# Performance work log

Hardware: AMD Instinct MI355X
Metric: run time of the kernel (lower is better)

The kernel has to match this reference:

```python
import jax, jax.numpy as jnp
import numpy as np

ALPHA = 1.0


def setup_inputs() -> dict:
    key = jax.random.key(0)
    k1, k2 = jax.random.split(key)
    N, K, D = 131072, 512, 512
    inputs = jax.random.normal(k1, (N, D), dtype=jnp.float32)
    # xavier-uniform style init for clusters
    limit = float(np.sqrt(6.0 / (K + D)))
    clusters = jax.random.uniform(k2, (K, D), dtype=jnp.float32, minval=-limit, maxval=limit)
    return {"inputs": inputs, "clusters": clusters}


def reference(inputs, clusters):
    # (same math as sum((x[:,None,:]-c)**2, -1), without the N x K x D intermediate)
    x2 = jnp.sum(inputs * inputs, axis=1, keepdims=True)          # [N, 1]
    c2 = jnp.sum(clusters * clusters, axis=1)[None, :]            # [1, K]
    d2 = jnp.maximum(x2 + c2 - 2.0 * (inputs @ clusters.T), 0.0)  # [N, K]
    q = 1.0 / (1.0 + d2 / ALPHA)
    q = q ** ((ALPHA + 1.0) / 2.0)
    return q / jnp.sum(q, axis=1, keepdims=True)
```

## Files before the change

kernel.cpp:

```cpp
#include <hip/hip_runtime.h>
#include <stdint.h>

#define NPTS 131072
#define DIM  512
#define KC   512
#define BM   32
#define BK   16
#define NKT  32

typedef float f32x16 __attribute__((ext_vector_type(16)));
typedef float f32x4  __attribute__((ext_vector_type(4)));
typedef float f32x2  __attribute__((ext_vector_type(2)));
typedef short bf16x8 __attribute__((ext_vector_type(8)));
typedef short bf16x2 __attribute__((ext_vector_type(2)));

__device__ __forceinline__ short f2bf(float f) {
  union { float f; unsigned u; } v; v.f = f;
  unsigned r = v.u + 0x7FFFu + ((v.u >> 16) & 1u);
  return (short)(r >> 16);
}

__device__ __forceinline__ bf16x8 pack8(f32x4 a, f32x4 b) {
  bf16x8 p;
  p[0] = f2bf(a.x); p[1] = f2bf(a.y); p[2] = f2bf(a.z); p[3] = f2bf(a.w);
  p[4] = f2bf(b.x); p[5] = f2bf(b.y); p[6] = f2bf(b.z); p[7] = f2bf(b.w);
  return p;
}

__device__ __forceinline__ float sq4(f32x4 a) {
  return a.x*a.x + a.y*a.y + a.z*a.z + a.w*a.w;
}

__device__ __forceinline__ void gload_lds16(const short* g, short* l) {
  __builtin_amdgcn_global_load_lds(
      (const __attribute__((address_space(1))) unsigned int*)g,
      (__attribute__((address_space(3))) unsigned int*)l, 16, 0, 0);
}

__global__ void dec_pack(const float* __restrict__ C, short* __restrict__ Bp,
                         float* __restrict__ c2) {
  const int n    = blockIdx.x;
  const int lane = threadIdx.x;
  const float* src = C + (size_t)n * DIM + lane * 8;
  f32x4 v0 = *(const f32x4*)src;
  f32x4 v1 = *(const f32x4*)(src + 4);
  float s = sq4(v0) + sq4(v1);
  #pragma unroll
  for (int m = 1; m < 64; m <<= 1) s += __shfl_xor(s, m, 64);
  if (lane == 0) c2[n] = s;
  const int kt = lane >> 1;
  const int h  = lane & 1;
  const int wn = n >> 7, nt = (n >> 5) & 3, r = n & 31;
  const size_t slot = ((size_t)(kt * 4 + wn) * 4 + nt) * 64 + h * 32 + r;
  *(bf16x8*)(Bp + slot * 8) = pack8(v0, v1);
}

__global__ __launch_bounds__(256, 4)
void dec_main(const float* __restrict__ X, const short* __restrict__ Bp,
              const float* __restrict__ c2g, float* __restrict__ out) {
  __shared__ short Bbuf[2][KC * BK];
  __shared__ short Abuf[2][BM * BK];
  __shared__ float x2sh[BM];
  __shared__ float part[4][BM];
  __shared__ float rowinv[BM];

  const int tid  = threadIdx.x;
  const int lane = tid & 63;
  const int wn   = tid >> 6;
  const int l31  = lane & 31;
  const int h    = lane >> 5;
  const int row0 = blockIdx.x * BM;

  const int arow = tid >> 3;
  const int acol = tid & 7;
  const float* aptr = X + (size_t)(row0 + arow) * DIM + acol * 2;
  const int awoff = (((acol >> 2) * 32 + arow) << 3) + ((acol & 3) << 1);

  const short* bsrc = Bp + tid * 8;

  f32x16 acc[4];
  #pragma unroll
  for (int nt = 0; nt < 4; ++nt) acc[nt] = (f32x16)0.f;
  float x2a = 0.f;

  {
    #pragma unroll
    for (int sw = 0; sw < 4; ++sw)
      gload_lds16(bsrc + sw * 2048, &Bbuf[0][sw * 2048 + tid * 8]);
    f32x2 a0 = *(const f32x2*)(aptr);
    x2a += a0.x * a0.x + a0.y * a0.y;
    bf16x2 p; p[0] = f2bf(a0.x); p[1] = f2bf(a0.y);
    *(bf16x2*)&Abuf[0][awoff] = p;
  }
  f32x2 av_w = *(const f32x2*)(aptr + 1 * BK);
  f32x2 av_p = *(const f32x2*)(aptr + 2 * BK);
  __syncthreads();

  #pragma unroll 2
  for (int kt = 0; kt < NKT; ++kt) {
    const int cur = kt & 1, nxt = cur ^ 1;

    if (kt + 1 < NKT) {
      #pragma unroll
      for (int sw = 0; sw < 4; ++sw)
        gload_lds16(bsrc + (size_t)(kt + 1) * 8192 + sw * 2048,
                    &Bbuf[nxt][sw * 2048 + tid * 8]);
      x2a += av_w.x * av_w.x + av_w.y * av_w.y;
      bf16x2 p; p[0] = f2bf(av_w.x); p[1] = f2bf(av_w.y);
      *(bf16x2*)&Abuf[nxt][awoff] = p;
      av_w = av_p;
      const int kpre = (kt + 3 < NKT) ? (kt + 3) : (NKT - 1);
      av_p = *(const f32x2*)(aptr + kpre * BK);
    }

    bf16x8 af = *(const bf16x8*)&Abuf[cur][lane * 8];
    bf16x8 bfr[4];
    #pragma unroll
    for (int nt = 0; nt < 4; ++nt)
      bfr[nt] = *(const bf16x8*)&Bbuf[cur][(wn * 4 + nt) * 512 + lane * 8];

    #pragma unroll
    for (int nt = 0; nt < 4; ++nt)
      acc[nt] = __builtin_amdgcn_mfma_f32_32x32x16_bf16(af, bfr[nt], acc[nt], 0, 0, 0);

    __syncthreads();
  }

  x2a += __shfl_xor(x2a, 1, 64);
  x2a += __shfl_xor(x2a, 2, 64);
  x2a += __shfl_xor(x2a, 4, 64);
  if ((tid & 7) == 0) x2sh[arow] = x2a;
  __syncthreads();

  float c2v[4];
  #pragma unroll
  for (int nt = 0; nt < 4; ++nt) c2v[nt] = c2g[wn * 128 + nt * 32 + l31];

  float srow[16];
  #pragma unroll
  for (int r = 0; r < 16; ++r) {
    const int row = (r & 3) + 8 * (r >> 2) + 4 * h;
    const float x2m = x2sh[row];
    float s = 0.f;
    #pragma unroll
    for (int nt = 0; nt < 4; ++nt) {
      float d2 = fmaxf(x2m + c2v[nt] - 2.f * acc[nt][r], 0.f);
      float q = __builtin_amdgcn_rcpf(1.f + d2);
      acc[nt][r] = q;
      s += q;
    }
    #pragma unroll
    for (int msk = 1; msk < 32; msk <<= 1) s += __shfl_xor(s, msk, 64);
    srow[r] = s;
  }

  if (l31 == 0) {
    #pragma unroll
    for (int r = 0; r < 16; ++r)
      part[wn][(r & 3) + 8 * (r >> 2) + 4 * h] = srow[r];
  }
  __syncthreads();
  if (tid < BM)
    rowinv[tid] = __builtin_amdgcn_rcpf(part[0][tid] + part[1][tid] +
                                        part[2][tid] + part[3][tid]);
  __syncthreads();

  #pragma unroll
  for (int r = 0; r < 16; ++r) {
    const int row = (r & 3) + 8 * (r >> 2) + 4 * h;
    const float iv = rowinv[row];
    float* o = out + (size_t)(row0 + row) * KC + wn * 128 + l31;
    #pragma unroll
    for (int nt = 0; nt < 4; ++nt)
      o[nt * 32] = acc[nt][r] * iv;
  }
}

extern "C" void kernel_launch(void* const* d_in, const int* in_sizes, int n_in,
                              void* d_out, int out_size, void* d_ws, size_t ws_size,
                              hipStream_t stream) {
  const float* X = (const float*)d_in[0];
  const float* C = (const float*)d_in[1];
  float* out = (float*)d_out;

  short* Bp = (short*)d_ws;
  float* c2 = (float*)((char*)d_ws + (size_t)KC * DIM * 2);

  dec_pack<<<KC, 64, 0, stream>>>(C, Bp, c2);
  dec_main<<<NPTS / BM, 256, 0, stream>>>(X, Bp, c2, out);
}
```

Measured before the change: 203.4 us.

## Double row tile and K step with 8 waves sharing each cluster tile

Raises the block tile from 32 to 64 rows using 512 threads arranged as 2x4 waves, so each staged cluster tile in LDS feeds twice as many rows. The K step doubles to 32 (two MFMA sub-steps per iteration), which halves the number of barriers. The packed cluster layout and the A-tile layout are reworked to match, and X loads become 16-byte vectors. LDS per block doubles to about 64KB, which may reduce occupancy below the launch-bounds target.

```diff
diff --git a/kernel.cpp b/kernel.cpp
--- a/kernel.cpp
+++ b/kernel.cpp
@@ -4,15 +4,14 @@
 #define NPTS 131072
 #define DIM  512
 #define KC   512
-#define BM   32
-#define BK   16
-#define NKT  32
+#define BM   64
+#define BK   32
+#define NKT  16
 
 typedef float f32x16 __attribute__((ext_vector_type(16)));
 typedef float f32x4  __attribute__((ext_vector_type(4)));
-typedef float f32x2  __attribute__((ext_vector_type(2)));
 typedef short bf16x8 __attribute__((ext_vector_type(8)));
-typedef short bf16x2 __attribute__((ext_vector_type(2)));
+typedef short bf16x4 __attribute__((ext_vector_type(4)));
 
 __device__ __forceinline__ short f2bf(float f) {
   union { float f; unsigned u; } v; v.f = f;
@@ -24,6 +23,12 @@
   bf16x8 p;
   p[0] = f2bf(a.x); p[1] = f2bf(a.y); p[2] = f2bf(a.z); p[3] = f2bf(a.w);
   p[4] = f2bf(b.x); p[5] = f2bf(b.y); p[6] = f2bf(b.z); p[7] = f2bf(b.w);
+  return p;
+}
+
+__device__ __forceinline__ bf16x4 pack4(f32x4 a) {
+  bf16x4 p;
+  p[0] = f2bf(a.x); p[1] = f2bf(a.y); p[2] = f2bf(a.z); p[3] = f2bf(a.w);
   return p;
 }
 
@@ -48,33 +53,38 @@
   #pragma unroll
   for (int m = 1; m < 64; m <<= 1) s += __shfl_xor(s, m, 64);
   if (lane == 0) c2[n] = s;
-  const int kt = lane >> 1;
-  const int h  = lane & 1;
+  const int kt = lane >> 2;
+  const int st = (lane >> 1) & 1;
+  const int hh = lane & 1;
   const int wn = n >> 7, nt = (n >> 5) & 3, r = n & 31;
-  const size_t slot = ((size_t)(kt * 4 + wn) * 4 + nt) * 64 + h * 32 + r;
+  const size_t slot =
+      (((size_t)(kt * 2 + st) * 4 + wn) * 4 + nt) * 64 + hh * 32 + r;
   *(bf16x8*)(Bp + slot * 8) = pack8(v0, v1);
 }
 
-__global__ __launch_bounds__(256, 4)
+__global__ __launch_bounds__(512, 4)
 void dec_main(const float* __restrict__ X, const short* __restrict__ Bp,
               const float* __restrict__ c2g, float* __restrict__ out) {
   __shared__ short Bbuf[2][KC * BK];
-  __shared__ short Abuf[2][BM * BK];
+  __shared__ short Abuf[2][2 * 2 * BM * 8];
   __shared__ float x2sh[BM];
   __shared__ float part[4][BM];
   __shared__ float rowinv[BM];
 
   const int tid  = threadIdx.x;
   const int lane = tid & 63;
-  const int wn   = tid >> 6;
+  const int wave = tid >> 6;
+  const int wm   = wave >> 2;
+  const int wn   = wave & 3;
   const int l31  = lane & 31;
   const int h    = lane >> 5;
   const int row0 = blockIdx.x * BM;
 
   const int arow = tid >> 3;
-  const int acol = tid & 7;
-  const float* aptr = X + (size_t)(row0 + arow) * DIM + acol * 2;
-  const int awoff = (((acol >> 2) * 32 + arow) << 3) + ((acol & 3) << 1);
+  const int ac   = tid & 7;
+  const float* aptr = X + (size_t)(row0 + arow) * DIM + ac * 4;
+  const int awoff = (((ac >> 2) * 2 + ((ac >> 1) & 1)) * BM + arow) * 8 +
+                    (ac & 1) * 4;
 
   const short* bsrc = Bp + tid * 8;
 
@@ -86,42 +96,45 @@
   {
     #pragma unroll
     for (int sw = 0; sw < 4; ++sw)
-      gload_lds16(bsrc + sw * 2048, &Bbuf[0][sw * 2048 + tid * 8]);
-    f32x2 a0 = *(const f32x2*)(aptr);
-    x2a += a0.x * a0.x + a0.y * a0.y;
-    bf16x2 p; p[0] = f2bf(a0.x); p[1] = f2bf(a0.y);
-    *(bf16x2*)&Abuf[0][awoff] = p;
-  }
-  f32x2 av_w = *(const f32x2*)(aptr + 1 * BK);
-  f32x2 av_p = *(const f32x2*)(aptr + 2 * BK);
-  __syncthreads();
-
-  #pragma unroll 2
+      gload_lds16(bsrc + sw * 4096, &Bbuf[0][sw * 4096 + tid * 8]);
+    f32x4 a0 = *(const f32x4*)(aptr);
+    x2a += sq4(a0);
+    *(bf16x4*)&Abuf[0][awoff] = pack4(a0);
+  }
+  f32x4 av_w = *(const f32x4*)(aptr + 1 * BK);
+  f32x4 av_p = *(const f32x4*)(aptr + 2 * BK);
+  __syncthreads();
+
   for (int kt = 0; kt < NKT; ++kt) {
     const int cur = kt & 1, nxt = cur ^ 1;
 
     if (kt + 1 < NKT) {
+      const int kpre = (kt + 3 < NKT) ? (kt + 3) : (NKT - 1);
+      f32x4 av_n = *(const f32x4*)(aptr + kpre * BK);
       #pragma unroll
       for (int sw = 0; sw < 4; ++sw)
-        gload_lds16(bsrc + (size_t)(kt + 1) * 8192 + sw * 2048,
-                    &Bbuf[nxt][sw * 2048 + tid * 8]);
-      x2a += av_w.x * av_w.x + av_w.y * av_w.y;
-      bf16x2 p; p[0] = f2bf(av_w.x); p[1] = f2bf(av_w.y);
-      *(bf16x2*)&Abuf[nxt][awoff] = p;
+        gload_lds16(bsrc + (size_t)(kt + 1) * 16384 + sw * 4096,
+                    &Bbuf[nxt][sw * 4096 + tid * 8]);
+      x2a += sq4(av_w);
+      *(bf16x4*)&Abuf[nxt][awoff] = pack4(av_w);
       av_w = av_p;
-      const int kpre = (kt + 3 < NKT) ? (kt + 3) : (NKT - 1);
-      av_p = *(const f32x2*)(aptr + kpre * BK);
+      av_p = av_n;
     }
 
-    bf16x8 af = *(const bf16x8*)&Abuf[cur][lane * 8];
-    bf16x8 bfr[4];
-    #pragma unroll
-    for (int nt = 0; nt < 4; ++nt)
-      bfr[nt] = *(const bf16x8*)&Bbuf[cur][(wn * 4 + nt) * 512 + lane * 8];
-
-    #pragma unroll
-    for (int nt = 0; nt < 4; ++nt)
-      acc[nt] = __builtin_amdgcn_mfma_f32_32x32x16_bf16(af, bfr[nt], acc[nt], 0, 0, 0);
+    #pragma unroll
+    for (int s = 0; s < 2; ++s) {
+      bf16x8 af = *(const bf16x8*)
+          &Abuf[cur][((s * 2 + h) * BM + wm * 32 + l31) * 8];
+      bf16x8 bfr[4];
+      #pragma unroll
+      for (int nt = 0; nt < 4; ++nt)
+        bfr[nt] = *(const bf16x8*)
+            &Bbuf[cur][((s * 4 + wn) * 4 + nt) * 512 + lane * 8];
+      #pragma unroll
+      for (int nt = 0; nt < 4; ++nt)
+        acc[nt] = __builtin_amdgcn_mfma_f32_32x32x16_bf16(
+            af, bfr[nt], acc[nt], 0, 0, 0);
+    }
 
     __syncthreads();
   }
@@ -139,8 +152,8 @@
   float srow[16];
   #pragma unroll
   for (int r = 0; r < 16; ++r) {
-    const int row = (r & 3) + 8 * (r >> 2) + 4 * h;
-    const float x2m = x2sh[row];
+    const int mloc = (r & 3) + 8 * (r >> 2) + 4 * h;
+    const float x2m = x2sh[wm * 32 + mloc];
     float s = 0.f;
     #pragma unroll
     for (int nt = 0; nt < 4; ++nt) {
@@ -157,7 +170,7 @@
   if (l31 == 0) {
     #pragma unroll
     for (int r = 0; r < 16; ++r)
-      part[wn][(r & 3) + 8 * (r >> 2) + 4 * h] = srow[r];
+      part[wn][wm * 32 + (r & 3) + 8 * (r >> 2) + 4 * h] = srow[r];
   }
   __syncthreads();
   if (tid < BM)
@@ -167,7 +180,7 @@
 
   #pragma unroll
   for (int r = 0; r < 16; ++r) {
-    const int row = (r & 3) + 8 * (r >> 2) + 4 * h;
+    const int row = wm * 32 + (r & 3) + 8 * (r >> 2) + 4 * h;
     const float iv = rowinv[row];
     float* o = out + (size_t)(row0 + row) * KC + wn * 128 + l31;
     #pragma unroll
@@ -187,5 +200,5 @@
   float* c2 = (float*)((char*)d_ws + (size_t)KC * DIM * 2);
 
   dec_pack<<<KC, 64, 0, stream>>>(C, Bp, c2);
-  dec_main<<<NPTS / BM, 256, 0, stream>>>(X, Bp, c2, out);
-}
+  dec_main<<<NPTS / BM, 512, 0, stream>>>(X, Bp, c2, out);
+}
```

Result: faster. 177.5 us (-12.7%).
